# Optimization experiments

Measured on AMD Instinct MI355X. Metric: run time of the kernel, lower is better.

The kernel has to match this reference:

```python
import jax, jax.numpy as jnp
import numpy as np

IN_DIMS = 512
TOKEN_DIM = 512
NUM_HEADS = 1
D = TOKEN_DIM * NUM_HEADS
SCALE = TOKEN_DIM ** (-0.5)
EPS = 1e-12  # torch F.normalize default


def _l2norm(v, axis):
    n = jnp.sqrt(jnp.sum(v * v, axis=axis, keepdims=True))
    return v / jnp.maximum(n, EPS)


def setup_inputs() -> dict:
    key = jax.random.key(0)
    ks = jax.random.split(key, 10)
    B, C, H, W = 64, IN_DIMS, 28, 28
    s_in = IN_DIMS ** -0.5
    s_d = D ** -0.5
    return {
        "x": jax.random.normal(ks[0], (B, C, H, W), jnp.float32),
        "Wq": jax.random.normal(ks[1], (IN_DIMS, D), jnp.float32) * s_in,
        "bq": jax.random.normal(ks[2], (D,), jnp.float32) * 0.01,
        "Wk": jax.random.normal(ks[3], (IN_DIMS, D), jnp.float32) * s_in,
        "bk": jax.random.normal(ks[4], (D,), jnp.float32) * 0.01,
        "w_g": jax.random.normal(ks[5], (D, 1), jnp.float32),
        "Wp": jax.random.normal(ks[6], (D, D), jnp.float32) * s_d,
        "bp": jax.random.normal(ks[7], (D,), jnp.float32) * 0.01,
        "Wf": jax.random.normal(ks[8], (D, TOKEN_DIM), jnp.float32) * s_d,
        "bf": jax.random.normal(ks[9], (TOKEN_DIM,), jnp.float32) * 0.01,
    }


def reference(x, Wq, bq, Wk, bk, w_g, Wp, bp, Wf, bf):
    B, C, H, W = x.shape
    t = x.reshape(B, C, H * W).transpose(0, 2, 1)          # [B, N, C]
    query = _l2norm(t @ Wq + bq, axis=-1)                  # [B, N, D]
    k = _l2norm(t @ Wk + bk, axis=-1)                      # [B, N, D]
    attn = _l2norm((query @ w_g) * SCALE, axis=1)          # [B, N, 1], normalized over tokens
    ctx = jnp.sum(attn * query, axis=1, keepdims=True)     # [B, 1, D] global context
    out = (ctx * k) @ Wp + bp + query                      # [B, N, D]
    out = out @ Wf + bf                                    # [B, N, TOKEN_DIM]
    return out.transpose(0, 2, 1).reshape(B, -1, H, W)
```

## Files before the change

kernel.cpp:

```cpp
#include <hip/hip_runtime.h>

#define EPSN 1e-12f
#define SCALE_F 0.044194173824159216f
#define MTOT 50176

typedef __bf16 bf16x8 __attribute__((ext_vector_type(8)));
typedef float  f32x4  __attribute__((ext_vector_type(4)));

__device__ __forceinline__ void gld16(const void* src, void* dst) {
  __builtin_amdgcn_global_load_lds(
      (const __attribute__((address_space(1))) unsigned int*)src,
      (__attribute__((address_space(3))) unsigned int*)dst, 16, 0, 0);
}

__global__ __launch_bounds__(256) void k_xt(const float* __restrict__ x,
                                            __bf16* __restrict__ xT, int b0) {
  __shared__ float T[32][33];
  const int n0 = blockIdx.x * 32, c0 = blockIdx.y * 32;
  const int bl = blockIdx.z, b = b0 + bl;
  const int dx = threadIdx.x, ty = threadIdx.y;
  #pragma unroll
  for (int pp = 0; pp < 4; ++pp) {
    int c = ty + pp * 8;
    int n = n0 + dx;
    T[c][dx] = (n < 784) ? x[((size_t)b * 512 + c0 + c) * 784 + n] : 0.f;
  }
  __syncthreads();
  #pragma unroll
  for (int pp = 0; pp < 4; ++pp) {
    int n = ty + pp * 8;
    if (n0 + n < 784)
      xT[((size_t)bl * 784 + n0 + n) * 512 + c0 + dx] = (__bf16)T[dx][n];
  }
}

__global__ __launch_bounds__(256) void k_prep_t(const float* __restrict__ Wq,
                                                const float* __restrict__ Wk,
                                                __bf16* __restrict__ WqT,
                                                __bf16* __restrict__ WkT) {
  __shared__ float Tq[32][33], Tk[32][33];
  const int c0 = blockIdx.x * 32, d0 = blockIdx.y * 32;
  const int dx = threadIdx.x, cy = threadIdx.y;
  #pragma unroll
  for (int p = 0; p < 4; ++p) {
    int c = cy + p * 8;
    Tq[c][dx] = Wq[(size_t)(c0 + c) * 512 + d0 + dx];
    Tk[c][dx] = Wk[(size_t)(c0 + c) * 512 + d0 + dx];
  }
  __syncthreads();
  #pragma unroll
  for (int p = 0; p < 4; ++p) {
    int d = cy + p * 8;
    WqT[(size_t)(d0 + d) * 512 + c0 + dx] = (__bf16)Tq[dx][d];
    WkT[(size_t)(d0 + d) * 512 + c0 + dx] = (__bf16)Tk[dx][d];
  }
}

__global__ __launch_bounds__(512) void k_prep_w(const float* __restrict__ Wp,
                                                const float* __restrict__ Wf,
                                                const float* __restrict__ bp,
                                                const float* __restrict__ bfv,
                                                __bf16* __restrict__ WcT,
                                                float* __restrict__ bpf) {
  const int kk0 = blockIdx.x * 2;
  const int d = threadIdx.x;
  float acc0 = 0.f, acc1 = 0.f, bacc = 0.f;
  const bool dobp = (blockIdx.x == 0);
  for (int c = 0; c < 512; ++c) {
    float wf = Wf[(size_t)c * 512 + d];
    acc0 = fmaf(Wp[(size_t)kk0 * 512 + c],       wf, acc0);
    acc1 = fmaf(Wp[(size_t)(kk0 + 1) * 512 + c], wf, acc1);
    if (dobp) bacc = fmaf(bp[c], wf, bacc);
  }
  WcT[(size_t)d * 1024 + kk0]           = (__bf16)acc0;
  WcT[(size_t)d * 1024 + kk0 + 1]       = (__bf16)acc1;
  WcT[(size_t)d * 1024 + 512 + kk0]     = (__bf16)Wf[(size_t)kk0 * 512 + d];
  WcT[(size_t)d * 1024 + 512 + kk0 + 1] = (__bf16)Wf[(size_t)(kk0 + 1) * 512 + d];
  if (dobp) bpf[d] = bacc + bfv[d];
}

__global__ __launch_bounds__(256, 2) void k_gemm(const __bf16* __restrict__ xT,
                                                 const __bf16* __restrict__ WqT,
                                                 const __bf16* __restrict__ WkT,
                                                 const float* __restrict__ bq,
                                                 const float* __restrict__ bk,
                                                 const float* __restrict__ wg,
                                                 const int b0,
                                                 __bf16* __restrict__ qraw,
                                                 __bf16* __restrict__ kraw,
                                                 float* __restrict__ psqQ,
                                                 float* __restrict__ psqK,
                                                 float* __restrict__ gdo) {
  __shared__ __align__(1024) unsigned char stg[3][24576];
  const int t = threadIdx.x, l = t & 63, w = t >> 6;
  const int li = l & 15, lq = l >> 4;
  const int p = blockIdx.x;
  const int xq = p & 7, q2 = p >> 3;
  const int nt = q2 & 3;
  const int g = (q2 >> 2) * 8 + xq;
  const int bl = g / 7, mt = g % 7;
  const int b = b0 + bl;
  const int m0 = mt * 128;

  const int r0 = 2 * w, r1 = r0 + 1;
  int row0 = m0 + r0 * 16 + li; if (row0 > 783) row0 = 783;
  int row1 = m0 + r1 * 16 + li; if (row1 > 783) row1 = 783;
  const __bf16* a0s = xT + ((size_t)bl * 784 + row0) * 512 + lq * 8;
  const __bf16* a1s = xT + ((size_t)bl * 784 + row1) * 512 + lq * 8;
  const __bf16* q0s = WqT + (size_t)(nt * 128 + r0 * 16 + li) * 512 + lq * 8;
  const __bf16* q1s = WqT + (size_t)(nt * 128 + r1 * 16 + li) * 512 + lq * 8;
  const __bf16* k0s = WkT + (size_t)(nt * 128 + r0 * 16 + li) * 512 + lq * 8;
  const __bf16* k1s = WkT + (size_t)(nt * 128 + r1 * 16 + li) * 512 + lq * 8;

  f32x4 accQ[4][4] = {}, accK[4][4] = {};

  auto stage = [&](unsigned char* buf, int ks) {
    const int kk = (ks > 15 ? 15 : ks) * 32;
    gld16(a0s + kk, buf + r0 * 1024);
    gld16(a1s + kk, buf + r1 * 1024);
    gld16(q0s + kk, buf + 8192 + r0 * 1024);
    gld16(q1s + kk, buf + 8192 + r1 * 1024);
    gld16(k0s + kk, buf + 16384 + r0 * 1024);
    gld16(k1s + kk, buf + 16384 + r1 * 1024);
  };
  auto mstep = [&](const unsigned char* buf) {
    bf16x8 af[4];
    #pragma unroll
    for (int rb = 0; rb < 4; ++rb)
      af[rb] = *(const bf16x8*)(buf + ((w & 1) * 4 + rb) * 1024 + l * 16);
    #pragma unroll
    for (int cb = 0; cb < 4; ++cb) {
      bf16x8 bq8 = *(const bf16x8*)(buf + 8192 + ((w >> 1) * 4 + cb) * 1024 + l * 16);
      #pragma unroll
      for (int rb = 0; rb < 4; ++rb)
        accQ[rb][cb] = __builtin_amdgcn_mfma_f32_16x16x32_bf16(af[rb], bq8, accQ[rb][cb], 0, 0, 0);
      bf16x8 bk8 = *(const bf16x8*)(buf + 16384 + ((w >> 1) * 4 + cb) * 1024 + l * 16);
      #pragma unroll
      for (int rb = 0; rb < 4; ++rb)
        accK[rb][cb] = __builtin_amdgcn_mfma_f32_16x16x32_bf16(af[rb], bk8, accK[rb][cb], 0, 0, 0);
    }
  };

  unsigned char *bc = stg[0], *bn = stg[1], *bn2 = stg[2];
  stage(bc, 0); stage(bn, 1);
  asm volatile("s_waitcnt vmcnt(6)" ::: "memory");
  __builtin_amdgcn_s_barrier();
  __builtin_amdgcn_sched_barrier(0);
  #pragma unroll 1
  for (int ks = 0; ks < 16; ++ks) {
    stage(bn2, ks + 2);
    __builtin_amdgcn_sched_barrier(0);
    mstep(bc);
    asm volatile("s_waitcnt vmcnt(6)" ::: "memory");
    __builtin_amdgcn_s_barrier();
    __builtin_amdgcn_sched_barrier(0);
    unsigned char* tmp = bc; bc = bn; bn = bn2; bn2 = tmp;
  }
  asm volatile("s_waitcnt vmcnt(0)" ::: "memory");

  const int colb = nt * 128 + (w >> 1) * 64;
  const int cg = nt * 2 + (w >> 1);
  float bqv[4], bkv[4], wv[4];
  #pragma unroll
  for (int cb = 0; cb < 4; ++cb) {
    int col = colb + cb * 16 + li;
    bqv[cb] = bq[col]; bkv[cb] = bk[col]; wv[cb] = wg[col];
  }
  #pragma unroll
  for (int rb = 0; rb < 4; ++rb)
    #pragma unroll
    for (int j = 0; j < 4; ++j) {
      int rowg = m0 + (w & 1) * 64 + rb * 16 + lq * 4 + j;
      bool ok = rowg < 784;
      size_t token = (size_t)b * 784 + rowg;
      float ssq = 0.f, ssk = 0.f, sg = 0.f;
      #pragma unroll
      for (int cb = 0; cb < 4; ++cb) {
        float vq = accQ[rb][cb][j] + bqv[cb];
        float vk = accK[rb][cb][j] + bkv[cb];
        ssq = fmaf(vq, vq, ssq);
        ssk = fmaf(vk, vk, ssk);
        sg  = fmaf(vq, wv[cb], sg);
        if (ok) {
          qraw[token * 512 + colb + cb * 16 + li] = (__bf16)vq;
          kraw[token * 512 + colb + cb * 16 + li] = (__bf16)vk;
        }
      }
      ssq += __shfl_xor(ssq, 1); ssq += __shfl_xor(ssq, 2); ssq += __shfl_xor(ssq, 4); ssq += __shfl_xor(ssq, 8);
      ssk += __shfl_xor(ssk, 1); ssk += __shfl_xor(ssk, 2); ssk += __shfl_xor(ssk, 4); ssk += __shfl_xor(ssk, 8);
      sg  += __shfl_xor(sg, 1);  sg  += __shfl_xor(sg, 2);  sg  += __shfl_xor(sg, 4);  sg  += __shfl_xor(sg, 8);
      if (ok && li == 0) {
        psqQ[(size_t)cg * MTOT + token] = ssq;
        psqK[(size_t)cg * MTOT + token] = ssk;
        gdo [(size_t)cg * MTOT + token] = sg;
      }
    }
}

__global__ __launch_bounds__(256) void k_normc(const float* __restrict__ psqQ,
                                               const float* __restrict__ psqK,
                                               const float* __restrict__ gdo,
                                               float* __restrict__ invqA,
                                               float* __restrict__ invkA,
                                               float* __restrict__ gA) {
  const int tkn = blockIdx.x * 256 + threadIdx.x;
  if (tkn >= MTOT) return;
  float sq = 0.f, sk = 0.f, gd = 0.f;
  #pragma unroll
  for (int cg = 0; cg < 8; ++cg) {
    sq += psqQ[(size_t)cg * MTOT + tkn];
    sk += psqK[(size_t)cg * MTOT + tkn];
    gd += gdo[(size_t)cg * MTOT + tkn];
  }
  float invq = 1.f / fmaxf(sqrtf(sq), EPSN);
  float invk = 1.f / fmaxf(sqrtf(sk), EPSN);
  invqA[tkn] = invq;
  invkA[tkn] = invk;
  gA[tkn]    = gd * invq;
}

__global__ __launch_bounds__(512) void k_scaleQ(__bf16* __restrict__ qraw,
                                                const float* __restrict__ invqA) {
  const int b = blockIdx.y;
  const int chunk = blockIdx.x * 512 + threadIdx.x;
  const int row = chunk >> 6;
  const int c8 = (chunk & 63) * 8;
  const size_t token = (size_t)b * 784 + row;
  __bf16* p = qraw + token * 512 + c8;
  const float s = invqA[token];
  bf16x8 v = *(const bf16x8*)p;
  #pragma unroll
  for (int j = 0; j < 8; ++j) v[j] = (__bf16)((float)v[j] * s);
  *(bf16x8*)p = v;
}

__global__ __launch_bounds__(512) void k_pctx(const __bf16* __restrict__ qn,
                                              const float* __restrict__ gA,
                                              float* __restrict__ ctx) {
  __shared__ float wred[8];
  __shared__ float part[4][128];
  const int ch = blockIdx.x, b = blockIdx.y, t = threadIdx.x;
  const size_t base = (size_t)b * 784;
  float gsq;
  { float gv = gA[base + t]; gsq = gv * gv; }
  if (t + 512 < 784) { float gv = gA[base + t + 512]; gsq = fmaf(gv, gv, gsq); }
  gsq += __shfl_xor(gsq, 1);  gsq += __shfl_xor(gsq, 2);  gsq += __shfl_xor(gsq, 4);
  gsq += __shfl_xor(gsq, 8);  gsq += __shfl_xor(gsq, 16); gsq += __shfl_xor(gsq, 32);
  if ((t & 63) == 0) wred[t >> 6] = gsq;
  __syncthreads();
  float tot = 0.f;
  #pragma unroll
  for (int i = 0; i < 8; ++i) tot += wred[i];
  const float alpha = SCALE_F / fmaxf(sqrtf(tot) * SCALE_F, EPSN);
  const int dof = t & 127, s = t >> 7;
  const int nb = s * 196;
  const __bf16* qb = qn + (base + nb) * 512 + ch * 128 + dof;
  const float* cf = gA + base + nb;
  float a0 = 0.f, a1 = 0.f, a2 = 0.f, a3 = 0.f;
  for (int n = 0; n < 196; n += 4) {
    a0 = fmaf(cf[n],     (float)qb[(size_t)n * 512],       a0);
    a1 = fmaf(cf[n + 1], (float)qb[(size_t)(n + 1) * 512], a1);
    a2 = fmaf(cf[n + 2], (float)qb[(size_t)(n + 2) * 512], a2);
    a3 = fmaf(cf[n + 3], (float)qb[(size_t)(n + 3) * 512], a3);
  }
  part[s][dof] = (a0 + a1) + (a2 + a3);
  __syncthreads();
  if (t < 128) {
    float sum = part[0][t] + part[1][t] + part[2][t] + part[3][t];
    ctx[(size_t)b * 512 + ch * 128 + t] = alpha * sum;
  }
}

__global__ __launch_bounds__(512) void k_scaleK(__bf16* __restrict__ kraw,
                                                const float* __restrict__ invkA,
                                                const float* __restrict__ ctx) {
  const int b = blockIdx.y;
  const int chunk = blockIdx.x * 512 + threadIdx.x;
  const int row = chunk >> 6;
  const int c8 = (chunk & 63) * 8;
  const size_t token = (size_t)b * 784 + row;
  __bf16* p = kraw + token * 512 + c8;
  const float s = invkA[token];
  f32x4 c0 = *(const f32x4*)(ctx + (size_t)b * 512 + c8);
  f32x4 c1 = *(const f32x4*)(ctx + (size_t)b * 512 + c8 + 4);
  bf16x8 v = *(const bf16x8*)p;
  #pragma unroll
  for (int j = 0; j < 4; ++j) {
    v[j]     = (__bf16)((float)v[j]     * s * c0[j]);
    v[4 + j] = (__bf16)((float)v[4 + j] * s * c1[j]);
  }
  *(bf16x8*)p = v;
}

__global__ __launch_bounds__(256, 3) void k_out(const __bf16* __restrict__ qn,
                                                const __bf16* __restrict__ kc,
                                                const __bf16* __restrict__ WcT,
                                                const float* __restrict__ bpf,
                                                float* __restrict__ out) {
  __shared__ __align__(1024) unsigned char stg[3][16384];
  const int t = threadIdx.x, l = t & 63, w = t >> 6;
  const int li = l & 15, lq = l >> 4;
  const int p = blockIdx.x;
  const int xq = p & 7, q2 = p >> 3;
  const int nt = q2 & 3;
  const int g = (q2 >> 2) * 8 + xq;
  const int b = g / 7, mt = g % 7;
  const int m0 = mt * 128;

  const int r0 = 2 * w, r1 = r0 + 1;
  int row0 = m0 + r0 * 16 + li; if (row0 > 783) row0 = 783;
  int row1 = m0 + r1 * 16 + li; if (row1 > 783) row1 = 783;
  const size_t tk0 = (size_t)b * 784 + row0, tk1 = (size_t)b * 784 + row1;
  const __bf16* ak0 = kc + tk0 * 512 + lq * 8;
  const __bf16* ak1 = kc + tk1 * 512 + lq * 8;
  const __bf16* aq0 = qn + tk0 * 512 + lq * 8;
  const __bf16* aq1 = qn + tk1 * 512 + lq * 8;
  const __bf16* wpB0 = WcT + (size_t)(nt * 128 + r0 * 16 + li) * 1024 + lq * 8;
  const __bf16* wpB1 = WcT + (size_t)(nt * 128 + r1 * 16 + li) * 1024 + lq * 8;

  f32x4 acc[4][4] = {};

  auto stage = [&](unsigned char* buf, int ks) {
    const int kk = ks > 31 ? 31 : ks;
    const int off = (kk & 15) * 32;
    const __bf16* s0 = (kk < 16) ? ak0 : aq0;
    const __bf16* s1 = (kk < 16) ? ak1 : aq1;
    gld16(s0 + off, buf + r0 * 1024);
    gld16(s1 + off, buf + r1 * 1024);
    gld16(wpB0 + kk * 32, buf + 8192 + r0 * 1024);
    gld16(wpB1 + kk * 32, buf + 8192 + r1 * 1024);
  };
  auto mstep = [&](const unsigned char* buf) {
    bf16x8 af[4];
    #pragma unroll
    for (int rb = 0; rb < 4; ++rb)
      af[rb] = *(const bf16x8*)(buf + ((w & 1) * 4 + rb) * 1024 + l * 16);
    #pragma unroll
    for (int cb = 0; cb < 4; ++cb) {
      bf16x8 bf = *(const bf16x8*)(buf + 8192 + ((w >> 1) * 4 + cb) * 1024 + l * 16);
      #pragma unroll
      for (int rb = 0; rb < 4; ++rb)
        acc[rb][cb] = __builtin_amdgcn_mfma_f32_16x16x32_bf16(af[rb], bf, acc[rb][cb], 0, 0, 0);
    }
  };

  unsigned char *bc = stg[0], *bn = stg[1], *bn2 = stg[2];
  stage(bc, 0); stage(bn, 1);
  asm volatile("s_waitcnt vmcnt(4)" ::: "memory");
  __builtin_amdgcn_s_barrier();
  __builtin_amdgcn_sched_barrier(0);
  #pragma unroll 1
  for (int ks = 0; ks < 32; ++ks) {
    stage(bn2, ks + 2);
    __builtin_amdgcn_sched_barrier(0);
    mstep(bc);
    asm volatile("s_waitcnt vmcnt(4)" ::: "memory");
    __builtin_amdgcn_s_barrier();
    __builtin_amdgcn_sched_barrier(0);
    unsigned char* tmp = bc; bc = bn; bn = bn2; bn2 = tmp;
  }
  asm volatile("s_waitcnt vmcnt(0)" ::: "memory");

  const int colb = nt * 128 + (w >> 1) * 64;
  float bv[4];
  #pragma unroll
  for (int cb = 0; cb < 4; ++cb) bv[cb] = bpf[colb + cb * 16 + li];
  #pragma unroll
  for (int rb = 0; rb < 4; ++rb) {
    int nrow = m0 + (w & 1) * 64 + rb * 16 + lq * 4;
    if (nrow < 784) {
      #pragma unroll
      for (int cb = 0; cb < 4; ++cb) {
        f32x4 v;
        #pragma unroll
        for (int j = 0; j < 4; ++j) v[j] = acc[rb][cb][j] + bv[cb];
        *(f32x4*)&out[((size_t)b * 512 + colb + cb * 16 + li) * 784 + nrow] = v;
      }
    }
  }
}

extern "C" void kernel_launch(void* const* d_in, const int* in_sizes, int n_in,
                              void* d_out, int out_size, void* d_ws, size_t ws_size,
                              hipStream_t stream) {
  const float* x   = (const float*)d_in[0];
  const float* Wq  = (const float*)d_in[1];
  const float* bq  = (const float*)d_in[2];
  const float* Wk  = (const float*)d_in[3];
  const float* bk  = (const float*)d_in[4];
  const float* wg  = (const float*)d_in[5];
  const float* Wp  = (const float*)d_in[6];
  const float* bp  = (const float*)d_in[7];
  const float* Wf  = (const float*)d_in[8];
  const float* bfv = (const float*)d_in[9];
  float* out = (float*)d_out;
  char* ws = (char*)d_ws;

  const size_t SZRAW = (size_t)MTOT * 512 * 2;
  const size_t SZXT  = (size_t)32 * 784 * 512 * 2;
  size_t off = 0;
  __bf16* qraw = (__bf16*)(ws + off); off += SZRAW;
  __bf16* kraw = (__bf16*)(ws + off); off += SZRAW;
  __bf16* xT   = (__bf16*)(ws + off); off += SZXT;
  __bf16* WqT  = (__bf16*)(ws + off); off += 524288;
  __bf16* WkT  = (__bf16*)(ws + off); off += 524288;
  __bf16* WcT  = (__bf16*)(ws + off); off += 1048576;
  float*  bpf  = (float*) (ws + off); off += 2048;
  float*  psqQ = (float*) (ws + off); off += (size_t)8 * MTOT * 4;
  float*  psqK = (float*) (ws + off); off += (size_t)8 * MTOT * 4;
  float*  gdo  = (float*) (ws + off); off += (size_t)8 * MTOT * 4;
  float*  invqA = (float*)(ws + off); off += (size_t)MTOT * 4;
  float*  invkA = (float*)(ws + off); off += (size_t)MTOT * 4;
  float*  gA    = (float*)(ws + off); off += (size_t)MTOT * 4;
  float*  ctx   = (float*)(ws + off); off += 131072;

  k_prep_t<<<dim3(16, 16), dim3(32, 8), 0, stream>>>(Wq, Wk, WqT, WkT);
  k_prep_w<<<dim3(256),    dim3(512),   0, stream>>>(Wp, Wf, bp, bfv, WcT, bpf);
  for (int s = 0; s < 2; ++s) {
    k_xt  <<<dim3(25, 16, 32), dim3(32, 8), 0, stream>>>(x, xT, s * 32);
    k_gemm<<<dim3(896),        dim3(256),   0, stream>>>(xT, WqT, WkT, bq, bk, wg, s * 32,
                                                         qraw, kraw, psqQ, psqK, gdo);
  }
  k_normc <<<dim3(196),    dim3(256), 0, stream>>>(psqQ, psqK, gdo, invqA, invkA, gA);
  k_scaleQ<<<dim3(98, 64), dim3(512), 0, stream>>>(qraw, invqA);
  k_pctx  <<<dim3(4, 64),  dim3(512), 0, stream>>>(qraw, gA, ctx);
  k_scaleK<<<dim3(98, 64), dim3(512), 0, stream>>>(kraw, invkA, ctx);
  k_out   <<<dim3(1792),   dim3(256), 0, stream>>>(qraw, kraw, WcT, bpf, out);
}
```

Baseline: 421.5 us.

## Fold L2-norm scaling into GEMM epilogue and per-batch context weights, drop scale passes

Removes the separate k_scaleQ/k_scaleK passes over the bf16 Q and K buffers. The per-token norms are applied as row scales inside the output GEMM (a ratio after the K half, inv-q at the end). The context vector is folded into a per-batch scaled copy of the combined weight matrix (k_wcb), so the K half of the GEMM uses a per-batch B operand. The QK GEMM is also split into separate Q and K blocks with smaller LDS and higher occupancy, and the two batch halves are merged into one launch. The trade-off is extra per-batch weight traffic (64 × 512 KB) and changed rounding from scaling raw bf16 values.

```diff
diff --git a/kernel.cpp b/kernel.cpp
--- a/kernel.cpp
+++ b/kernel.cpp
@@ -14,10 +14,10 @@
 }
 
 __global__ __launch_bounds__(256) void k_xt(const float* __restrict__ x,
-                                            __bf16* __restrict__ xT, int b0) {
+                                            __bf16* __restrict__ xT) {
   __shared__ float T[32][33];
   const int n0 = blockIdx.x * 32, c0 = blockIdx.y * 32;
-  const int bl = blockIdx.z, b = b0 + bl;
+  const int b = blockIdx.z;
   const int dx = threadIdx.x, ty = threadIdx.y;
   #pragma unroll
   for (int pp = 0; pp < 4; ++pp) {
@@ -30,7 +30,7 @@
   for (int pp = 0; pp < 4; ++pp) {
     int n = ty + pp * 8;
     if (n0 + n < 784)
-      xT[((size_t)bl * 784 + n0 + n) * 512 + c0 + dx] = (__bf16)T[dx][n];
+      xT[((size_t)b * 784 + n0 + n) * 512 + c0 + dx] = (__bf16)T[dx][n];
   }
 }
 
@@ -79,49 +79,45 @@
   if (dobp) bpf[d] = bacc + bfv[d];
 }
 
-__global__ __launch_bounds__(256, 2) void k_gemm(const __bf16* __restrict__ xT,
+__global__ __launch_bounds__(256, 3) void k_gemm(const __bf16* __restrict__ xT,
                                                  const __bf16* __restrict__ WqT,
                                                  const __bf16* __restrict__ WkT,
                                                  const float* __restrict__ bq,
                                                  const float* __restrict__ bk,
                                                  const float* __restrict__ wg,
-                                                 const int b0,
                                                  __bf16* __restrict__ qraw,
                                                  __bf16* __restrict__ kraw,
                                                  float* __restrict__ psqQ,
                                                  float* __restrict__ psqK,
                                                  float* __restrict__ gdo) {
-  __shared__ __align__(1024) unsigned char stg[3][24576];
+  __shared__ __align__(1024) unsigned char stg[3][16384];
   const int t = threadIdx.x, l = t & 63, w = t >> 6;
   const int li = l & 15, lq = l >> 4;
   const int p = blockIdx.x;
   const int xq = p & 7, q2 = p >> 3;
-  const int nt = q2 & 3;
-  const int g = (q2 >> 2) * 8 + xq;
-  const int bl = g / 7, mt = g % 7;
-  const int b = b0 + bl;
+  const int m8 = q2 & 7;
+  const int g = (q2 >> 3) * 8 + xq;
+  const int b = g / 7, mt = g % 7;
+  const int qk = m8 >> 2, nt = m8 & 3;
   const int m0 = mt * 128;
+  const __bf16* Wt = qk ? WkT : WqT;
 
   const int r0 = 2 * w, r1 = r0 + 1;
   int row0 = m0 + r0 * 16 + li; if (row0 > 783) row0 = 783;
   int row1 = m0 + r1 * 16 + li; if (row1 > 783) row1 = 783;
-  const __bf16* a0s = xT + ((size_t)bl * 784 + row0) * 512 + lq * 8;
-  const __bf16* a1s = xT + ((size_t)bl * 784 + row1) * 512 + lq * 8;
-  const __bf16* q0s = WqT + (size_t)(nt * 128 + r0 * 16 + li) * 512 + lq * 8;
-  const __bf16* q1s = WqT + (size_t)(nt * 128 + r1 * 16 + li) * 512 + lq * 8;
-  const __bf16* k0s = WkT + (size_t)(nt * 128 + r0 * 16 + li) * 512 + lq * 8;
-  const __bf16* k1s = WkT + (size_t)(nt * 128 + r1 * 16 + li) * 512 + lq * 8;
-
-  f32x4 accQ[4][4] = {}, accK[4][4] = {};
+  const __bf16* a0s = xT + ((size_t)b * 784 + row0) * 512 + lq * 8;
+  const __bf16* a1s = xT + ((size_t)b * 784 + row1) * 512 + lq * 8;
+  const __bf16* w0s = Wt + (size_t)(nt * 128 + r0 * 16 + li) * 512 + lq * 8;
+  const __bf16* w1s = Wt + (size_t)(nt * 128 + r1 * 16 + li) * 512 + lq * 8;
+
+  f32x4 acc[4][4] = {};
 
   auto stage = [&](unsigned char* buf, int ks) {
     const int kk = (ks > 15 ? 15 : ks) * 32;
     gld16(a0s + kk, buf + r0 * 1024);
     gld16(a1s + kk, buf + r1 * 1024);
-    gld16(q0s + kk, buf + 8192 + r0 * 1024);
-    gld16(q1s + kk, buf + 8192 + r1 * 1024);
-    gld16(k0s + kk, buf + 16384 + r0 * 1024);
-    gld16(k1s + kk, buf + 16384 + r1 * 1024);
+    gld16(w0s + kk, buf + 8192 + r0 * 1024);
+    gld16(w1s + kk, buf + 8192 + r1 * 1024);
   };
   auto mstep = [&](const unsigned char* buf) {
     bf16x8 af[4];
@@ -130,20 +126,16 @@
       af[rb] = *(const bf16x8*)(buf + ((w & 1) * 4 + rb) * 1024 + l * 16);
     #pragma unroll
     for (int cb = 0; cb < 4; ++cb) {
-      bf16x8 bq8 = *(const bf16x8*)(buf + 8192 + ((w >> 1) * 4 + cb) * 1024 + l * 16);
+      bf16x8 bf = *(const bf16x8*)(buf + 8192 + ((w >> 1) * 4 + cb) * 1024 + l * 16);
       #pragma unroll
       for (int rb = 0; rb < 4; ++rb)
-        accQ[rb][cb] = __builtin_amdgcn_mfma_f32_16x16x32_bf16(af[rb], bq8, accQ[rb][cb], 0, 0, 0);
-      bf16x8 bk8 = *(const bf16x8*)(buf + 16384 + ((w >> 1) * 4 + cb) * 1024 + l * 16);
-      #pragma unroll
-      for (int rb = 0; rb < 4; ++rb)
-        accK[rb][cb] = __builtin_amdgcn_mfma_f32_16x16x32_bf16(af[rb], bk8, accK[rb][cb], 0, 0, 0);
+        acc[rb][cb] = __builtin_amdgcn_mfma_f32_16x16x32_bf16(af[rb], bf, acc[rb][cb], 0, 0, 0);
     }
   };
 
   unsigned char *bc = stg[0], *bn = stg[1], *bn2 = stg[2];
   stage(bc, 0); stage(bn, 1);
-  asm volatile("s_waitcnt vmcnt(6)" ::: "memory");
+  asm volatile("s_waitcnt vmcnt(4)" ::: "memory");
   __builtin_amdgcn_s_barrier();
   __builtin_amdgcn_sched_barrier(0);
   #pragma unroll 1
@@ -151,20 +143,24 @@
     stage(bn2, ks + 2);
     __builtin_amdgcn_sched_barrier(0);
     mstep(bc);
-    asm volatile("s_waitcnt vmcnt(6)" ::: "memory");
+    asm volatile("s_waitcnt vmcnt(4)" ::: "memory");
     __builtin_amdgcn_s_barrier();
     __builtin_amdgcn_sched_barrier(0);
     unsigned char* tmp = bc; bc = bn; bn = bn2; bn2 = tmp;
   }
   asm volatile("s_waitcnt vmcnt(0)" ::: "memory");
 
+  const float* bias = qk ? bk : bq;
+  __bf16* dst = qk ? kraw : qraw;
+  float* psq = qk ? psqK : psqQ;
   const int colb = nt * 128 + (w >> 1) * 64;
   const int cg = nt * 2 + (w >> 1);
-  float bqv[4], bkv[4], wv[4];
+  float bv[4], wv[4];
   #pragma unroll
   for (int cb = 0; cb < 4; ++cb) {
     int col = colb + cb * 16 + li;
-    bqv[cb] = bq[col]; bkv[cb] = bk[col]; wv[cb] = wg[col];
+    bv[cb] = bias[col];
+    wv[cb] = qk ? 0.f : wg[col];
   }
   #pragma unroll
   for (int rb = 0; rb < 4; ++rb)
@@ -173,26 +169,19 @@
       int rowg = m0 + (w & 1) * 64 + rb * 16 + lq * 4 + j;
       bool ok = rowg < 784;
       size_t token = (size_t)b * 784 + rowg;
-      float ssq = 0.f, ssk = 0.f, sg = 0.f;
+      float ss = 0.f, sg = 0.f;
       #pragma unroll
       for (int cb = 0; cb < 4; ++cb) {
-        float vq = accQ[rb][cb][j] + bqv[cb];
-        float vk = accK[rb][cb][j] + bkv[cb];
-        ssq = fmaf(vq, vq, ssq);
-        ssk = fmaf(vk, vk, ssk);
-        sg  = fmaf(vq, wv[cb], sg);
-        if (ok) {
-          qraw[token * 512 + colb + cb * 16 + li] = (__bf16)vq;
-          kraw[token * 512 + colb + cb * 16 + li] = (__bf16)vk;
-        }
+        float v = acc[rb][cb][j] + bv[cb];
+        ss = fmaf(v, v, ss);
+        sg = fmaf(v, wv[cb], sg);
+        if (ok) dst[token * 512 + colb + cb * 16 + li] = (__bf16)v;
       }
-      ssq += __shfl_xor(ssq, 1); ssq += __shfl_xor(ssq, 2); ssq += __shfl_xor(ssq, 4); ssq += __shfl_xor(ssq, 8);
-      ssk += __shfl_xor(ssk, 1); ssk += __shfl_xor(ssk, 2); ssk += __shfl_xor(ssk, 4); ssk += __shfl_xor(ssk, 8);
-      sg  += __shfl_xor(sg, 1);  sg  += __shfl_xor(sg, 2);  sg  += __shfl_xor(sg, 4);  sg  += __shfl_xor(sg, 8);
+      ss += __shfl_xor(ss, 1); ss += __shfl_xor(ss, 2); ss += __shfl_xor(ss, 4); ss += __shfl_xor(ss, 8);
+      sg += __shfl_xor(sg, 1); sg += __shfl_xor(sg, 2); sg += __shfl_xor(sg, 4); sg += __shfl_xor(sg, 8);
       if (ok && li == 0) {
-        psqQ[(size_t)cg * MTOT + token] = ssq;
-        psqK[(size_t)cg * MTOT + token] = ssk;
-        gdo [(size_t)cg * MTOT + token] = sg;
+        psq[(size_t)cg * MTOT + token] = ss;
+        if (!qk) gdo[(size_t)cg * MTOT + token] = sg;
       }
     }
 }
@@ -201,7 +190,8 @@
                                                const float* __restrict__ psqK,
                                                const float* __restrict__ gdo,
                                                float* __restrict__ invqA,
-                                               float* __restrict__ invkA,
+                                               float* __restrict__ ratioA,
+                                               float* __restrict__ coefA,
                                                float* __restrict__ gA) {
   const int tkn = blockIdx.x * 256 + threadIdx.x;
   if (tkn >= MTOT) return;
@@ -212,29 +202,18 @@
     sk += psqK[(size_t)cg * MTOT + tkn];
     gd += gdo[(size_t)cg * MTOT + tkn];
   }
-  float invq = 1.f / fmaxf(sqrtf(sq), EPSN);
-  float invk = 1.f / fmaxf(sqrtf(sk), EPSN);
-  invqA[tkn] = invq;
-  invkA[tkn] = invk;
-  gA[tkn]    = gd * invq;
-}
-
-__global__ __launch_bounds__(512) void k_scaleQ(__bf16* __restrict__ qraw,
-                                                const float* __restrict__ invqA) {
-  const int b = blockIdx.y;
-  const int chunk = blockIdx.x * 512 + threadIdx.x;
-  const int row = chunk >> 6;
-  const int c8 = (chunk & 63) * 8;
-  const size_t token = (size_t)b * 784 + row;
-  __bf16* p = qraw + token * 512 + c8;
-  const float s = invqA[token];
-  bf16x8 v = *(const bf16x8*)p;
-  #pragma unroll
-  for (int j = 0; j < 8; ++j) v[j] = (__bf16)((float)v[j] * s);
-  *(bf16x8*)p = v;
-}
-
-__global__ __launch_bounds__(512) void k_pctx(const __bf16* __restrict__ qn,
+  float nq = fmaxf(sqrtf(sq), EPSN);
+  float nk = fmaxf(sqrtf(sk), EPSN);
+  float invq = 1.f / nq;
+  float gv = gd * invq;
+  invqA[tkn]  = invq;
+  ratioA[tkn] = nq / nk;
+  coefA[tkn]  = gv * invq;
+  gA[tkn]     = gv;
+}
+
+__global__ __launch_bounds__(512) void k_pctx(const __bf16* __restrict__ qraw,
+                                              const float* __restrict__ coefA,
                                               const float* __restrict__ gA,
                                               float* __restrict__ ctx) {
   __shared__ float wred[8];
@@ -254,8 +233,8 @@
   const float alpha = SCALE_F / fmaxf(sqrtf(tot) * SCALE_F, EPSN);
   const int dof = t & 127, s = t >> 7;
   const int nb = s * 196;
-  const __bf16* qb = qn + (base + nb) * 512 + ch * 128 + dof;
-  const float* cf = gA + base + nb;
+  const __bf16* qb = qraw + (base + nb) * 512 + ch * 128 + dof;
+  const float* cf = coefA + base + nb;
   float a0 = 0.f, a1 = 0.f, a2 = 0.f, a3 = 0.f;
   for (int n = 0; n < 196; n += 4) {
     a0 = fmaf(cf[n],     (float)qb[(size_t)n * 512],       a0);
@@ -271,30 +250,30 @@
   }
 }
 
-__global__ __launch_bounds__(512) void k_scaleK(__bf16* __restrict__ kraw,
-                                                const float* __restrict__ invkA,
-                                                const float* __restrict__ ctx) {
+__global__ __launch_bounds__(256) void k_wcb(const __bf16* __restrict__ WcT,
+                                             const float* __restrict__ ctx,
+                                             __bf16* __restrict__ Bc) {
   const int b = blockIdx.y;
-  const int chunk = blockIdx.x * 512 + threadIdx.x;
-  const int row = chunk >> 6;
-  const int c8 = (chunk & 63) * 8;
-  const size_t token = (size_t)b * 784 + row;
-  __bf16* p = kraw + token * 512 + c8;
-  const float s = invkA[token];
-  f32x4 c0 = *(const f32x4*)(ctx + (size_t)b * 512 + c8);
-  f32x4 c1 = *(const f32x4*)(ctx + (size_t)b * 512 + c8 + 4);
-  bf16x8 v = *(const bf16x8*)p;
+  const int idx = (blockIdx.x * 256 + threadIdx.x) * 8;
+  const int d = idx >> 9, k = idx & 511;
+  bf16x8 wv = *(const bf16x8*)(WcT + (size_t)d * 1024 + k);
+  f32x4 c0 = *(const f32x4*)(ctx + (size_t)b * 512 + k);
+  f32x4 c1 = *(const f32x4*)(ctx + (size_t)b * 512 + k + 4);
+  bf16x8 r;
   #pragma unroll
   for (int j = 0; j < 4; ++j) {
-    v[j]     = (__bf16)((float)v[j]     * s * c0[j]);
-    v[4 + j] = (__bf16)((float)v[4 + j] * s * c1[j]);
-  }
-  *(bf16x8*)p = v;
-}
-
-__global__ __launch_bounds__(256, 3) void k_out(const __bf16* __restrict__ qn,
-                                                const __bf16* __restrict__ kc,
+    r[j]     = (__bf16)((float)wv[j]     * c0[j]);
+    r[4 + j] = (__bf16)((float)wv[4 + j] * c1[j]);
+  }
+  *(bf16x8*)(Bc + ((size_t)b << 18) + idx) = r;
+}
+
+__global__ __launch_bounds__(256, 3) void k_out(const __bf16* __restrict__ qraw,
+                                                const __bf16* __restrict__ kraw,
+                                                const __bf16* __restrict__ Bc,
                                                 const __bf16* __restrict__ WcT,
+                                                const float* __restrict__ invqA,
+                                                const float* __restrict__ ratioA,
                                                 const float* __restrict__ bpf,
                                                 float* __restrict__ out) {
   __shared__ __align__(1024) unsigned char stg[3][16384];
@@ -311,24 +290,43 @@
   int row0 = m0 + r0 * 16 + li; if (row0 > 783) row0 = 783;
   int row1 = m0 + r1 * 16 + li; if (row1 > 783) row1 = 783;
   const size_t tk0 = (size_t)b * 784 + row0, tk1 = (size_t)b * 784 + row1;
-  const __bf16* ak0 = kc + tk0 * 512 + lq * 8;
-  const __bf16* ak1 = kc + tk1 * 512 + lq * 8;
-  const __bf16* aq0 = qn + tk0 * 512 + lq * 8;
-  const __bf16* aq1 = qn + tk1 * 512 + lq * 8;
-  const __bf16* wpB0 = WcT + (size_t)(nt * 128 + r0 * 16 + li) * 1024 + lq * 8;
-  const __bf16* wpB1 = WcT + (size_t)(nt * 128 + r1 * 16 + li) * 1024 + lq * 8;
+  const __bf16* ak0 = kraw + tk0 * 512 + lq * 8;
+  const __bf16* ak1 = kraw + tk1 * 512 + lq * 8;
+  const __bf16* aq0 = qraw + tk0 * 512 + lq * 8;
+  const __bf16* aq1 = qraw + tk1 * 512 + lq * 8;
+  const __bf16* bc0 = Bc + ((size_t)b << 18) + (size_t)(nt * 128 + r0 * 16 + li) * 512 + lq * 8;
+  const __bf16* bc1 = Bc + ((size_t)b << 18) + (size_t)(nt * 128 + r1 * 16 + li) * 512 + lq * 8;
+  const __bf16* wp0 = WcT + (size_t)(nt * 128 + r0 * 16 + li) * 1024 + lq * 8;
+  const __bf16* wp1 = WcT + (size_t)(nt * 128 + r1 * 16 + li) * 1024 + lq * 8;
+
+  float ratio16[16], invq16[16];
+  #pragma unroll
+  for (int rb = 0; rb < 4; ++rb)
+    #pragma unroll
+    for (int j = 0; j < 4; ++j) {
+      int rowg = m0 + (w & 1) * 64 + rb * 16 + lq * 4 + j;
+      if (rowg > 783) rowg = 783;
+      size_t token = (size_t)b * 784 + rowg;
+      ratio16[rb * 4 + j] = ratioA[token];
+      invq16[rb * 4 + j]  = invqA[token];
+    }
 
   f32x4 acc[4][4] = {};
 
   auto stage = [&](unsigned char* buf, int ks) {
     const int kk = ks > 31 ? 31 : ks;
     const int off = (kk & 15) * 32;
-    const __bf16* s0 = (kk < 16) ? ak0 : aq0;
-    const __bf16* s1 = (kk < 16) ? ak1 : aq1;
-    gld16(s0 + off, buf + r0 * 1024);
-    gld16(s1 + off, buf + r1 * 1024);
-    gld16(wpB0 + kk * 32, buf + 8192 + r0 * 1024);
-    gld16(wpB1 + kk * 32, buf + 8192 + r1 * 1024);
+    if (kk < 16) {
+      gld16(ak0 + off, buf + r0 * 1024);
+      gld16(ak1 + off, buf + r1 * 1024);
+      gld16(bc0 + off, buf + 8192 + r0 * 1024);
+      gld16(bc1 + off, buf + 8192 + r1 * 1024);
+    } else {
+      gld16(aq0 + off, buf + r0 * 1024);
+      gld16(aq1 + off, buf + r1 * 1024);
+      gld16(wp0 + kk * 32, buf + 8192 + r0 * 1024);
+      gld16(wp1 + kk * 32, buf + 8192 + r1 * 1024);
+    }
   };
   auto mstep = [&](const unsigned char* buf) {
     bf16x8 af[4];
@@ -344,20 +342,37 @@
     }
   };
 
-  unsigned char *bc = stg[0], *bn = stg[1], *bn2 = stg[2];
-  stage(bc, 0); stage(bn, 1);
+  unsigned char *bc_ = stg[0], *bn = stg[1], *bn2 = stg[2];
+  stage(bc_, 0); stage(bn, 1);
   asm volatile("s_waitcnt vmcnt(4)" ::: "memory");
   __builtin_amdgcn_s_barrier();
   __builtin_amdgcn_sched_barrier(0);
   #pragma unroll 1
-  for (int ks = 0; ks < 32; ++ks) {
+  for (int ks = 0; ks < 16; ++ks) {
     stage(bn2, ks + 2);
     __builtin_amdgcn_sched_barrier(0);
-    mstep(bc);
+    mstep(bc_);
     asm volatile("s_waitcnt vmcnt(4)" ::: "memory");
     __builtin_amdgcn_s_barrier();
     __builtin_amdgcn_sched_barrier(0);
-    unsigned char* tmp = bc; bc = bn; bn = bn2; bn2 = tmp;
+    unsigned char* tmp = bc_; bc_ = bn; bn = bn2; bn2 = tmp;
+  }
+  #pragma unroll
+  for (int rb = 0; rb < 4; ++rb)
+    #pragma unroll
+    for (int cb = 0; cb < 4; ++cb)
+      #pragma unroll
+      for (int j = 0; j < 4; ++j)
+        acc[rb][cb][j] *= ratio16[rb * 4 + j];
+  #pragma unroll 1
+  for (int ks = 16; ks < 32; ++ks) {
+    stage(bn2, ks + 2);
+    __builtin_amdgcn_sched_barrier(0);
+    mstep(bc_);
+    asm volatile("s_waitcnt vmcnt(4)" ::: "memory");
+    __builtin_amdgcn_s_barrier();
+    __builtin_amdgcn_sched_barrier(0);
+    unsigned char* tmp = bc_; bc_ = bn; bn = bn2; bn2 = tmp;
   }
   asm volatile("s_waitcnt vmcnt(0)" ::: "memory");
 
@@ -373,7 +388,8 @@
       for (int cb = 0; cb < 4; ++cb) {
         f32x4 v;
         #pragma unroll
-        for (int j = 0; j < 4; ++j) v[j] = acc[rb][cb][j] + bv[cb];
+        for (int j = 0; j < 4; ++j)
+          v[j] = acc[rb][cb][j] * invq16[rb * 4 + j] + bv[cb];
         *(f32x4*)&out[((size_t)b * 512 + colb + cb * 16 + li) * 784 + nrow] = v;
       }
     }
@@ -397,11 +413,11 @@
   char* ws = (char*)d_ws;
 
   const size_t SZRAW = (size_t)MTOT * 512 * 2;
-  const size_t SZXT  = (size_t)32 * 784 * 512 * 2;
   size_t off = 0;
   __bf16* qraw = (__bf16*)(ws + off); off += SZRAW;
   __bf16* kraw = (__bf16*)(ws + off); off += SZRAW;
-  __bf16* xT   = (__bf16*)(ws + off); off += SZXT;
+  __bf16* xT   = (__bf16*)(ws + off); off += SZRAW;
+  __bf16* Bc   = xT;
   __bf16* WqT  = (__bf16*)(ws + off); off += 524288;
   __bf16* WkT  = (__bf16*)(ws + off); off += 524288;
   __bf16* WcT  = (__bf16*)(ws + off); off += 1048576;
@@ -409,21 +425,20 @@
   float*  psqQ = (float*) (ws + off); off += (size_t)8 * MTOT * 4;
   float*  psqK = (float*) (ws + off); off += (size_t)8 * MTOT * 4;
   float*  gdo  = (float*) (ws + off); off += (size_t)8 * MTOT * 4;
-  float*  invqA = (float*)(ws + off); off += (size_t)MTOT * 4;
-  float*  invkA = (float*)(ws + off); off += (size_t)MTOT * 4;
-  float*  gA    = (float*)(ws + off); off += (size_t)MTOT * 4;
-  float*  ctx   = (float*)(ws + off); off += 131072;
-
-  k_prep_t<<<dim3(16, 16), dim3(32, 8), 0, stream>>>(Wq, Wk, WqT, WkT);
-  k_prep_w<<<dim3(256),    dim3(512),   0, stream>>>(Wp, Wf, bp, bfv, WcT, bpf);
-  for (int s = 0; s < 2; ++s) {
-    k_xt  <<<dim3(25, 16, 32), dim3(32, 8), 0, stream>>>(x, xT, s * 32);
-    k_gemm<<<dim3(896),        dim3(256),   0, stream>>>(xT, WqT, WkT, bq, bk, wg, s * 32,
+  float*  invqA  = (float*)(ws + off); off += (size_t)MTOT * 4;
+  float*  ratioA = (float*)(ws + off); off += (size_t)MTOT * 4;
+  float*  coefA  = (float*)(ws + off); off += (size_t)MTOT * 4;
+  float*  gA     = (float*)(ws + off); off += (size_t)MTOT * 4;
+  float*  ctx    = (float*)(ws + off); off += 131072;
+
+  k_prep_t<<<dim3(16, 16),     dim3(32, 8), 0, stream>>>(Wq, Wk, WqT, WkT);
+  k_prep_w<<<dim3(256),        dim3(512),   0, stream>>>(Wp, Wf, bp, bfv, WcT, bpf);
+  k_xt    <<<dim3(25, 16, 64), dim3(32, 8), 0, stream>>>(x, xT);
+  k_gemm  <<<dim3(3584),       dim3(256),   0, stream>>>(xT, WqT, WkT, bq, bk, wg,
                                                          qraw, kraw, psqQ, psqK, gdo);
-  }
-  k_normc <<<dim3(196),    dim3(256), 0, stream>>>(psqQ, psqK, gdo, invqA, invkA, gA);
-  k_scaleQ<<<dim3(98, 64), dim3(512), 0, stream>>>(qraw, invqA);
-  k_pctx  <<<dim3(4, 64),  dim3(512), 0, stream>>>(qraw, gA, ctx);
-  k_scaleK<<<dim3(98, 64), dim3(512), 0, stream>>>(kraw, invkA, ctx);
-  k_out   <<<dim3(1792),   dim3(256), 0, stream>>>(qraw, kraw, WcT, bpf, out);
-}
+  k_normc <<<dim3(196),        dim3(256),   0, stream>>>(psqQ, psqK, gdo, invqA, ratioA, coefA, gA);
+  k_pctx  <<<dim3(4, 64),      dim3(512),   0, stream>>>(qraw, coefA, gA, ctx);
+  k_wcb   <<<dim3(128, 64),    dim3(256),   0, stream>>>(WcT, ctx, Bc);
+  k_out   <<<dim3(1792),       dim3(256),   0, stream>>>(qraw, kraw, Bc, WcT, invqA, ratioA,
+                                                         bpf, out);
+}
```

Result: faster. 399.6 us (-5.2%).
